# Performance work log

Measured on AMD Instinct MI355X. Metric: run time of the kernel, lower is better.

## Reference

```python
import jax, jax.numpy as jnp
import numpy as np

B, N, DIM = 2, 2048, 512
HEADS, DIM_HEAD = 8, 64
INNER = HEADS * DIM_HEAD  # 512
SCALE = DIM_HEAD ** -0.5


def setup_inputs() -> dict:
    key = jax.random.key(0)
    k1, k2, k3, k4, k5 = jax.random.split(key, 5)
    s = 0.02
    return {
        "x1": jax.random.normal(k1, (B, N, DIM), jnp.float32),
        "x2": jax.random.normal(k2, (B, N, DIM), jnp.float32),
        "W_qk": jax.random.normal(k3, (DIM, 2 * INNER), jnp.float32) * s,
        "W_v": jax.random.normal(k4, (DIM, INNER), jnp.float32) * s,
        "W_out": jax.random.normal(k5, (INNER, DIM), jnp.float32) * s,
        "b_out": jnp.zeros((DIM,), jnp.float32),
    }


def _split_heads(t):
    # [b, n, h*d] -> [b, h, n, d]
    b, n, _ = t.shape
    return t.reshape(b, n, HEADS, DIM_HEAD).transpose(0, 2, 1, 3)


def reference(x1, x2, W_qk, W_v, W_out, b_out):
    # to_qk(x1) -> chunk into k, v ; to_v(x2) -> q  (names in orig are swapped)
    kv = x1 @ W_qk                      # [b, n1, 2*inner]
    k, v = jnp.split(kv, 2, axis=-1)
    q = x2 @ W_v                        # [b, n2, inner]
    q, k, v = _split_heads(q), _split_heads(k), _split_heads(v)  # [b,h,n,d]
    dots = jnp.einsum("bhid,bhjd->bhij", q, k) * SCALE  # [b,h,n2,n1]
    attn = jax.nn.softmax(dots, axis=-1)
    out = jnp.einsum("bhij,bhjd->bhid", attn, v)         # [b,h,n2,d]
    out = out.transpose(0, 2, 1, 3).reshape(out.shape[0], out.shape[2], INNER)
    return out @ W_out + b_out          # [b, n2, dim]
```

## Files before the change

kernel.cpp:

```cpp
#include <hip/hip_runtime.h>

typedef short bf16x8 __attribute__((ext_vector_type(8)));
typedef float f32x4 __attribute__((ext_vector_type(4)));
typedef unsigned short u16;
typedef u16 u16x8 __attribute__((ext_vector_type(8)));
typedef u16 u16x4 __attribute__((ext_vector_type(4)));

#define DEV __device__ __forceinline__

DEV u16 f2bf(float f) {
  unsigned u = __float_as_uint(f);
  u += 0x7fff + ((u >> 16) & 1);
  return (u16)(u >> 16);
}

#define MFMA16(a, b, c) __builtin_amdgcn_mfma_f32_16x16x32_bf16(a, b, c, 0, 0, 0)

__global__ __launch_bounds__(256) void preproc(
    const float* __restrict__ x1, const float* __restrict__ x2,
    const float* __restrict__ Wqk, const float* __restrict__ Wv,
    const float* __restrict__ Wout,
    u16* __restrict__ x1b, u16* __restrict__ x2b,
    u16* __restrict__ WqkT, u16* __restrict__ WvT, u16* __restrict__ WoutT) {
  __shared__ float tf[32][33];
  int bx = blockIdx.x, t = threadIdx.x;
  if (bx < 2048) {
    const float* src = (bx < 1024) ? x1 : x2;
    u16* dst = (bx < 1024) ? x1b : x2b;
    long base = (long)(bx & 1023) * 2048 + t * 8;
    float4 a = *(const float4*)(src + base);
    float4 b = *(const float4*)(src + base + 4);
    u16x8 o;
    o[0] = f2bf(a.x); o[1] = f2bf(a.y); o[2] = f2bf(a.z); o[3] = f2bf(a.w);
    o[4] = f2bf(b.x); o[5] = f2bf(b.y); o[6] = f2bf(b.z); o[7] = f2bf(b.w);
    *(u16x8*)(dst + base) = o;
    return;
  }
  const float* src; u16* dst; int Ncols; int id;
  if (bx < 2560)      { id = bx - 2048; src = Wqk;  dst = WqkT;  Ncols = 1024; }
  else if (bx < 2816) { id = bx - 2560; src = Wv;   dst = WvT;   Ncols = 512;  }
  else                { id = bx - 2816; src = Wout; dst = WoutT; Ncols = 512;  }
  int tilesPerRow = Ncols >> 5;
  int tr = id / tilesPerRow, tc = id % tilesPerRow;
  int r0 = tr * 32, c0 = tc * 32;
  {
    int r = t >> 3, c4 = (t & 7) * 4;
    float4 v = *(const float4*)(src + (long)(r0 + r) * Ncols + c0 + c4);
    tf[r][c4] = v.x; tf[r][c4 + 1] = v.y; tf[r][c4 + 2] = v.z; tf[r][c4 + 3] = v.w;
  }
  __syncthreads();
  {
    int c = t >> 3, r4 = (t & 7) * 4;
    u16x4 o;
    o[0] = f2bf(tf[r4][c]); o[1] = f2bf(tf[r4 + 1][c]);
    o[2] = f2bf(tf[r4 + 2][c]); o[3] = f2bf(tf[r4 + 3][c]);
    *(u16x4*)(dst + (long)(c0 + c) * 512 + r0 + r4) = o;
  }
}

template <int MODE>
__global__ __launch_bounds__(256) void gemm_bf16(
    const u16* __restrict__ A, const u16* __restrict__ BT,
    u16* __restrict__ out_q, u16* __restrict__ out_k, u16* __restrict__ out_v,
    float* __restrict__ out_f, const float* __restrict__ bias) {
  __shared__ u16 sA[2][128 * 40];
  __shared__ u16 sB[2][64 * 40];
  int t = threadIdx.x, bx = blockIdx.x;
  int m0 = (bx & 31) * 128, n0 = (bx >> 5) * 64;
  int w = t >> 6, l = t & 63, lm = l & 15, lq = l >> 4;

  f32x4 zero = {0.f, 0.f, 0.f, 0.f};
  f32x4 acc[2][4];
#pragma unroll
  for (int i = 0; i < 2; ++i)
#pragma unroll
    for (int j = 0; j < 4; ++j) acc[i][j] = zero;

  int sm = t >> 2;
  int skc = (t & 3) * 8;
  const u16* gA = A + (long)(m0 + sm) * 512 + skc;
  const u16* gB = BT + (long)(n0 + sm) * 512 + skc;

  bf16x8 a0 = *(const bf16x8*)(gA);
  bf16x8 a1 = *(const bf16x8*)(gA + (long)64 * 512);
  bf16x8 b0 = *(const bf16x8*)(gB);
  *(bf16x8*)(sA[0] + sm * 40 + skc) = a0;
  *(bf16x8*)(sA[0] + (sm + 64) * 40 + skc) = a1;
  *(bf16x8*)(sB[0] + sm * 40 + skc) = b0;
  __syncthreads();

  for (int kt = 0; kt < 16; ++kt) {
    int cur = kt & 1;
    if (kt < 15) {
      a0 = *(const bf16x8*)(gA + (kt + 1) * 32);
      a1 = *(const bf16x8*)(gA + (long)64 * 512 + (kt + 1) * 32);
      b0 = *(const bf16x8*)(gB + (kt + 1) * 32);
    }
    bf16x8 af[2], bfr[4];
    af[0] = *(const bf16x8*)(sA[cur] + (w * 32 + lm) * 40 + lq * 8);
    af[1] = *(const bf16x8*)(sA[cur] + (w * 32 + 16 + lm) * 40 + lq * 8);
#pragma unroll
    for (int s = 0; s < 4; ++s)
      bfr[s] = *(const bf16x8*)(sB[cur] + (s * 16 + lm) * 40 + lq * 8);
#pragma unroll
    for (int ms = 0; ms < 2; ++ms)
#pragma unroll
      for (int s = 0; s < 4; ++s)
        acc[ms][s] = MFMA16(af[ms], bfr[s], acc[ms][s]);
    if (kt < 15) {
      int nxt = 1 - cur;
      *(bf16x8*)(sA[nxt] + sm * 40 + skc) = a0;
      *(bf16x8*)(sA[nxt] + (sm + 64) * 40 + skc) = a1;
      *(bf16x8*)(sB[nxt] + sm * 40 + skc) = b0;
    }
    __syncthreads();
  }

#pragma unroll
  for (int ms = 0; ms < 2; ++ms) {
    int gmBase = m0 + w * 32 + ms * 16 + lq * 4;
#pragma unroll
    for (int s = 0; s < 4; ++s) {
      int gc = n0 + s * 16 + lm;
#pragma unroll
      for (int r = 0; r < 4; ++r) {
        int gm = gmBase + r;
        float v = acc[ms][s][r];
        if (MODE == 2) {
          out_f[(long)gm * 512 + gc] = v + bias[gc];
        } else if (MODE == 0) {
          int b = gm >> 11, n = gm & 2047;
          out_q[(((long)(b << 3) + (gc >> 6)) * 2048 + n) * 64 + (gc & 63)] =
              f2bf(v * 0.125f);
        } else {
          int b = gm >> 11, n = gm & 2047;
          if (gc < 512)
            out_k[(((long)(b << 3) + (gc >> 6)) * 2048 + n) * 64 + (gc & 63)] = f2bf(v);
          else {
            int c = gc - 512;
            out_v[(((long)(b << 3) + (c >> 6)) * 2048 + n) * 64 + (c & 63)] = f2bf(v);
          }
        }
      }
    }
  }
}

__global__ __launch_bounds__(256) void vtrans(const u16* __restrict__ V,
                                              u16* __restrict__ Vt) {
  __shared__ u16 tile[64][72];
  int nt = blockIdx.x, bh = blockIdx.y;
  const u16* src = V + ((long)bh * 2048 + nt * 64) * 64;
  u16* dst = Vt + (long)bh * 64 * 2048 + nt * 64;
  int t = threadIdx.x;
  int r = t >> 2, c = (t & 3) * 16;
  *(u16x8*)(&tile[r][c]) = *(const u16x8*)(src + (long)r * 64 + c);
  *(u16x8*)(&tile[r][c + 8]) = *(const u16x8*)(src + (long)r * 64 + c + 8);
  __syncthreads();
  int d = t >> 2, n0 = (t & 3) * 16;
  u16x8 o0, o1;
#pragma unroll
  for (int i = 0; i < 8; ++i) {
    o0[i] = tile[n0 + i][d];
    o1[i] = tile[n0 + 8 + i][d];
  }
  *(u16x8*)(dst + (long)d * 2048 + n0) = o0;
  *(u16x8*)(dst + (long)d * 2048 + n0 + 8) = o1;
}

__global__ __launch_bounds__(256) void attn(
    const u16* __restrict__ Q, const u16* __restrict__ K,
    const u16* __restrict__ Vt, u16* __restrict__ O) {
  int qt = blockIdx.x, bh = blockIdx.y;
  int b = bh >> 3, h = bh & 7;
  const u16* Kh = K + (long)bh * 2048 * 64;
  const u16* Vh = Vt + (long)bh * 64 * 2048;
  int t = threadIdx.x, w = t >> 6, l = t & 63, lm = l & 15, lq = l >> 4;

  __shared__ u16 sK[2][64 * 72];
  __shared__ u16 sV[2][64 * 72];
  __shared__ u16 sP[64 * 72];

  bf16x8 qf[2];
  {
    const u16* qptr = Q + (long)bh * 2048 * 64 + (long)(qt * 64 + w * 16 + lm) * 64 + lq * 8;
    qf[0] = *(const bf16x8*)(qptr);
    qf[1] = *(const bf16x8*)(qptr + 32);
  }

  f32x4 zero = {0.f, 0.f, 0.f, 0.f};
  f32x4 accO[4];
#pragma unroll
  for (int s = 0; s < 4; ++s) accO[s] = zero;
  f32x4 lacc = zero;

  int row = t >> 2, c16 = (t & 3) * 16;
  const u16* gK = Kh + (long)row * 64 + c16;
  const u16* gV = Vh + (long)row * 2048 + c16;

  bf16x8 k0 = *(const bf16x8*)(gK);
  bf16x8 k1 = *(const bf16x8*)(gK + 8);
  bf16x8 v0 = *(const bf16x8*)(gV);
  bf16x8 v1 = *(const bf16x8*)(gV + 8);
  *(bf16x8*)(sK[0] + row * 72 + c16) = k0;
  *(bf16x8*)(sK[0] + row * 72 + c16 + 8) = k1;
  *(bf16x8*)(sV[0] + row * 72 + c16) = v0;
  *(bf16x8*)(sV[0] + row * 72 + c16 + 8) = v1;
  __syncthreads();

  for (int jt = 0; jt < 32; ++jt) {
    int cur = jt & 1;
    if (jt < 31) {
      long off = (long)(jt + 1) * 64;
      k0 = *(const bf16x8*)(gK + off * 64);
      k1 = *(const bf16x8*)(gK + off * 64 + 8);
      v0 = *(const bf16x8*)(gV + off);
      v1 = *(const bf16x8*)(gV + off + 8);
    }
    const u16* bK = sK[cur];
    const u16* bV = sV[cur];

    f32x4 sacc[4];
#pragma unroll
    for (int s = 0; s < 4; ++s) sacc[s] = zero;
#pragma unroll
    for (int s = 0; s < 4; ++s) {
      bf16x8 kf0 = *(const bf16x8*)(bK + (s * 16 + lm) * 72 + lq * 8);
      bf16x8 kf1 = *(const bf16x8*)(bK + (s * 16 + lm) * 72 + 32 + lq * 8);
      sacc[s] = MFMA16(qf[0], kf0, sacc[s]);
      sacc[s] = MFMA16(qf[1], kf1, sacc[s]);
    }

    float p[4][4];
#pragma unroll
    for (int s = 0; s < 4; ++s)
#pragma unroll
      for (int r = 0; r < 4; ++r) {
        float e = __expf(sacc[s][r]);
        p[s][r] = e;
        lacc[r] += e;
      }

#pragma unroll
    for (int s = 0; s < 4; ++s)
#pragma unroll
      for (int r = 0; r < 4; ++r)
        sP[(w * 16 + lq * 4 + r) * 72 + s * 16 + lm] = f2bf(p[s][r]);

    bf16x8 pf0 = *(const bf16x8*)(sP + (w * 16 + lm) * 72 + lq * 8);
    bf16x8 pf1 = *(const bf16x8*)(sP + (w * 16 + lm) * 72 + 32 + lq * 8);
#pragma unroll
    for (int s = 0; s < 4; ++s) {
      bf16x8 vf0 = *(const bf16x8*)(bV + (s * 16 + lm) * 72 + lq * 8);
      bf16x8 vf1 = *(const bf16x8*)(bV + (s * 16 + lm) * 72 + 32 + lq * 8);
      accO[s] = MFMA16(pf0, vf0, accO[s]);
      accO[s] = MFMA16(pf1, vf1, accO[s]);
    }

    if (jt < 31) {
      int nxt = 1 - cur;
      *(bf16x8*)(sK[nxt] + row * 72 + c16) = k0;
      *(bf16x8*)(sK[nxt] + row * 72 + c16 + 8) = k1;
      *(bf16x8*)(sV[nxt] + row * 72 + c16) = v0;
      *(bf16x8*)(sV[nxt] + row * 72 + c16 + 8) = v1;
    }
    __syncthreads();
  }

#pragma unroll
  for (int m = 1; m < 16; m <<= 1) {
    lacc[0] += __shfl_xor(lacc[0], m);
    lacc[1] += __shfl_xor(lacc[1], m);
    lacc[2] += __shfl_xor(lacc[2], m);
    lacc[3] += __shfl_xor(lacc[3], m);
  }
  f32x4 inv;
#pragma unroll
  for (int r = 0; r < 4; ++r) inv[r] = 1.f / lacc[r];

#pragma unroll
  for (int s = 0; s < 4; ++s)
#pragma unroll
    for (int r = 0; r < 4; ++r) {
      int n = qt * 64 + w * 16 + lq * 4 + r;
      O[((long)b * 2048 + n) * 512 + h * 64 + s * 16 + lm] = f2bf(accO[s][r] * inv[r]);
    }
}

extern "C" void kernel_launch(void* const* d_in, const int* in_sizes, int n_in,
                              void* d_out, int out_size, void* d_ws, size_t ws_size,
                              hipStream_t stream) {
  const float* x1 = (const float*)d_in[0];
  const float* x2 = (const float*)d_in[1];
  const float* Wqk = (const float*)d_in[2];
  const float* Wv = (const float*)d_in[3];
  const float* Wout = (const float*)d_in[4];
  const float* bout = (const float*)d_in[5];
  float* out = (float*)d_out;

  u16* ws = (u16*)d_ws;
  const long SZ = 2097152;
  u16* Qw = ws;
  u16* Kw = ws + SZ;
  u16* Vw = ws + 2 * SZ;
  u16* Ow = ws + 3 * SZ;
  u16* x1b = ws + 4 * SZ;
  u16* x2b = ws + 5 * SZ;
  u16* Vtw = ws + 6 * SZ;
  u16* WqkT = ws + 7 * SZ;
  u16* WvT = ws + 7 * SZ + 524288;
  u16* WoutT = ws + 7 * SZ + 524288 + 262144;

  preproc<<<3072, 256, 0, stream>>>(x1, x2, Wqk, Wv, Wout, x1b, x2b, WqkT, WvT, WoutT);
  gemm_bf16<0><<<256, 256, 0, stream>>>(x2b, WvT, Qw, nullptr, nullptr, nullptr, nullptr);
  gemm_bf16<1><<<512, 256, 0, stream>>>(x1b, WqkT, nullptr, Kw, Vw, nullptr, nullptr);
  vtrans<<<dim3(32, 16), 256, 0, stream>>>(Vw, Vtw);
  attn<<<dim3(32, 16), 256, 0, stream>>>(Qw, Kw, Vtw, Ow);
  gemm_bf16<2><<<256, 256, 0, stream>>>(Ow, WoutT, nullptr, nullptr, nullptr, out, bout);
}
```

Before: 149.6 us.

## Fuse input conversion and V transpose into GEMMs, rework attention with 32x32 MFMA

The fp32-to-bf16 conversion of x1/x2 moves into the projection GEMM's A-operand loads, dropping a separate conversion pass and its workspace traffic. The KV GEMM writes V already transposed, which removes the vtrans kernel. The attention kernel is rewritten to use 32x32 MFMA tiles with 128-thread blocks and keeps P in registers, using the 32x32x8 MFMA layout or lane shuffles instead of an LDS round-trip. The trade-off is more register pressure and fewer waves per block in attention, plus uncoalesced 4-element strided stores for Vt.

```diff
diff --git a/kernel.cpp b/kernel.cpp
--- a/kernel.cpp
+++ b/kernel.cpp
@@ -1,7 +1,9 @@
 #include <hip/hip_runtime.h>
 
 typedef short bf16x8 __attribute__((ext_vector_type(8)));
+typedef short bf16x4 __attribute__((ext_vector_type(4)));
 typedef float f32x4 __attribute__((ext_vector_type(4)));
+typedef float f32x16 __attribute__((ext_vector_type(16)));
 typedef unsigned short u16;
 typedef u16 u16x8 __attribute__((ext_vector_type(8)));
 typedef u16 u16x4 __attribute__((ext_vector_type(4)));
@@ -14,32 +16,31 @@
   return (u16)(u >> 16);
 }
 
+DEV int pkbf(float lo, float hi) {
+  return __builtin_amdgcn_perm(__float_as_uint(hi) + 0x8000u,
+                               __float_as_uint(lo) + 0x8000u, 0x07060302u);
+}
+
 #define MFMA16(a, b, c) __builtin_amdgcn_mfma_f32_16x16x32_bf16(a, b, c, 0, 0, 0)
-
-__global__ __launch_bounds__(256) void preproc(
-    const float* __restrict__ x1, const float* __restrict__ x2,
+#define MFMA3216(a, b, c) __builtin_amdgcn_mfma_f32_32x32x16_bf16(a, b, c, 0, 0, 0)
+
+#if __has_builtin(__builtin_amdgcn_mfma_f32_32x32x8bf16_1k)
+#define HAVE_PV8 1
+#define PVMFMA(a, b, c) __builtin_amdgcn_mfma_f32_32x32x8bf16_1k(a, b, c, 0, 0, 0)
+#else
+#define HAVE_PV8 0
+#endif
+
+__global__ __launch_bounds__(256) void wprep(
     const float* __restrict__ Wqk, const float* __restrict__ Wv,
     const float* __restrict__ Wout,
-    u16* __restrict__ x1b, u16* __restrict__ x2b,
     u16* __restrict__ WqkT, u16* __restrict__ WvT, u16* __restrict__ WoutT) {
   __shared__ float tf[32][33];
   int bx = blockIdx.x, t = threadIdx.x;
-  if (bx < 2048) {
-    const float* src = (bx < 1024) ? x1 : x2;
-    u16* dst = (bx < 1024) ? x1b : x2b;
-    long base = (long)(bx & 1023) * 2048 + t * 8;
-    float4 a = *(const float4*)(src + base);
-    float4 b = *(const float4*)(src + base + 4);
-    u16x8 o;
-    o[0] = f2bf(a.x); o[1] = f2bf(a.y); o[2] = f2bf(a.z); o[3] = f2bf(a.w);
-    o[4] = f2bf(b.x); o[5] = f2bf(b.y); o[6] = f2bf(b.z); o[7] = f2bf(b.w);
-    *(u16x8*)(dst + base) = o;
-    return;
-  }
   const float* src; u16* dst; int Ncols; int id;
-  if (bx < 2560)      { id = bx - 2048; src = Wqk;  dst = WqkT;  Ncols = 1024; }
-  else if (bx < 2816) { id = bx - 2560; src = Wv;   dst = WvT;   Ncols = 512;  }
-  else                { id = bx - 2816; src = Wout; dst = WoutT; Ncols = 512;  }
+  if (bx < 512)      { id = bx;       src = Wqk;  dst = WqkT;  Ncols = 1024; }
+  else if (bx < 768) { id = bx - 512; src = Wv;   dst = WvT;   Ncols = 512; }
+  else               { id = bx - 768; src = Wout; dst = WoutT; Ncols = 512; }
   int tilesPerRow = Ncols >> 5;
   int tr = id / tilesPerRow, tc = id % tilesPerRow;
   int r0 = tr * 32, c0 = tc * 32;
@@ -59,10 +60,11 @@
 }
 
 template <int MODE>
-__global__ __launch_bounds__(256) void gemm_bf16(
-    const u16* __restrict__ A, const u16* __restrict__ BT,
-    u16* __restrict__ out_q, u16* __restrict__ out_k, u16* __restrict__ out_v,
+__global__ __launch_bounds__(256) void gemm_k(
+    const void* __restrict__ Ap, const u16* __restrict__ BT,
+    u16* __restrict__ out_q, u16* __restrict__ out_k, u16* __restrict__ out_vt,
     float* __restrict__ out_f, const float* __restrict__ bias) {
+  constexpr bool AF32 = (MODE != 2);
   __shared__ u16 sA[2][128 * 40];
   __shared__ u16 sB[2][64 * 40];
   int t = threadIdx.x, bx = blockIdx.x;
@@ -78,11 +80,28 @@
 
   int sm = t >> 2;
   int skc = (t & 3) * 8;
-  const u16* gA = A + (long)(m0 + sm) * 512 + skc;
+  const float* gAf = (const float*)Ap + (long)(m0 + sm) * 512 + skc;
+  const u16* gAh = (const u16*)Ap + (long)(m0 + sm) * 512 + skc;
   const u16* gB = BT + (long)(n0 + sm) * 512 + skc;
 
-  bf16x8 a0 = *(const bf16x8*)(gA);
-  bf16x8 a1 = *(const bf16x8*)(gA + (long)64 * 512);
+  auto loadA = [&](int kt, int rows) {
+    bf16x8 o;
+    long off = (long)rows * 512 + kt * 32;
+    if constexpr (AF32) {
+      float4 f0 = *(const float4*)(gAf + off);
+      float4 f1 = *(const float4*)(gAf + off + 4);
+      o[0] = (short)f2bf(f0.x); o[1] = (short)f2bf(f0.y);
+      o[2] = (short)f2bf(f0.z); o[3] = (short)f2bf(f0.w);
+      o[4] = (short)f2bf(f1.x); o[5] = (short)f2bf(f1.y);
+      o[6] = (short)f2bf(f1.z); o[7] = (short)f2bf(f1.w);
+    } else {
+      o = *(const bf16x8*)(gAh + off);
+    }
+    return o;
+  };
+
+  bf16x8 a0 = loadA(0, 0);
+  bf16x8 a1 = loadA(0, 64);
   bf16x8 b0 = *(const bf16x8*)(gB);
   *(bf16x8*)(sA[0] + sm * 40 + skc) = a0;
   *(bf16x8*)(sA[0] + (sm + 64) * 40 + skc) = a1;
@@ -92,8 +111,8 @@
   for (int kt = 0; kt < 16; ++kt) {
     int cur = kt & 1;
     if (kt < 15) {
-      a0 = *(const bf16x8*)(gA + (kt + 1) * 32);
-      a1 = *(const bf16x8*)(gA + (long)64 * 512 + (kt + 1) * 32);
+      a0 = loadA(kt + 1, 0);
+      a1 = loadA(kt + 1, 64);
       b0 = *(const bf16x8*)(gB + (kt + 1) * 32);
     }
     bf16x8 af[2], bfr[4];
@@ -122,168 +141,166 @@
 #pragma unroll
     for (int s = 0; s < 4; ++s) {
       int gc = n0 + s * 16 + lm;
-#pragma unroll
-      for (int r = 0; r < 4; ++r) {
-        int gm = gmBase + r;
-        float v = acc[ms][s][r];
-        if (MODE == 2) {
-          out_f[(long)gm * 512 + gc] = v + bias[gc];
-        } else if (MODE == 0) {
-          int b = gm >> 11, n = gm & 2047;
-          out_q[(((long)(b << 3) + (gc >> 6)) * 2048 + n) * 64 + (gc & 63)] =
-              f2bf(v * 0.125f);
+      if (MODE == 2) {
+#pragma unroll
+        for (int r = 0; r < 4; ++r)
+          out_f[(long)(gmBase + r) * 512 + gc] = acc[ms][s][r] + bias[gc];
+      } else if (MODE == 0) {
+        int b = gmBase >> 11, n = gmBase & 2047;
+#pragma unroll
+        for (int r = 0; r < 4; ++r)
+          out_q[(((long)(b << 3) + (gc >> 6)) * 2048 + n + r) * 64 + (gc & 63)] =
+              f2bf(acc[ms][s][r] * 0.125f);
+      } else {
+        int b = gmBase >> 11, n = gmBase & 2047;
+        if (gc < 512) {
+#pragma unroll
+          for (int r = 0; r < 4; ++r)
+            out_k[(((long)(b << 3) + (gc >> 6)) * 2048 + n + r) * 64 + (gc & 63)] =
+                f2bf(acc[ms][s][r]);
         } else {
-          int b = gm >> 11, n = gm & 2047;
-          if (gc < 512)
-            out_k[(((long)(b << 3) + (gc >> 6)) * 2048 + n) * 64 + (gc & 63)] = f2bf(v);
-          else {
-            int c = gc - 512;
-            out_v[(((long)(b << 3) + (c >> 6)) * 2048 + n) * 64 + (c & 63)] = f2bf(v);
-          }
+          int c = gc - 512, h = c >> 6, d = c & 63;
+          u16x4 vv;
+#pragma unroll
+          for (int r = 0; r < 4; ++r) vv[r] = f2bf(acc[ms][s][r]);
+          *(u16x4*)(out_vt + (((long)(b << 3) + h) * 64 + d) * 2048 + n) = vv;
         }
       }
     }
   }
 }
 
-__global__ __launch_bounds__(256) void vtrans(const u16* __restrict__ V,
-                                              u16* __restrict__ Vt) {
-  __shared__ u16 tile[64][72];
-  int nt = blockIdx.x, bh = blockIdx.y;
-  const u16* src = V + ((long)bh * 2048 + nt * 64) * 64;
-  u16* dst = Vt + (long)bh * 64 * 2048 + nt * 64;
-  int t = threadIdx.x;
-  int r = t >> 2, c = (t & 3) * 16;
-  *(u16x8*)(&tile[r][c]) = *(const u16x8*)(src + (long)r * 64 + c);
-  *(u16x8*)(&tile[r][c + 8]) = *(const u16x8*)(src + (long)r * 64 + c + 8);
-  __syncthreads();
-  int d = t >> 2, n0 = (t & 3) * 16;
-  u16x8 o0, o1;
-#pragma unroll
-  for (int i = 0; i < 8; ++i) {
-    o0[i] = tile[n0 + i][d];
-    o1[i] = tile[n0 + 8 + i][d];
-  }
-  *(u16x8*)(dst + (long)d * 2048 + n0) = o0;
-  *(u16x8*)(dst + (long)d * 2048 + n0 + 8) = o1;
-}
-
-__global__ __launch_bounds__(256) void attn(
+__global__ __launch_bounds__(128) void attn(
     const u16* __restrict__ Q, const u16* __restrict__ K,
     const u16* __restrict__ Vt, u16* __restrict__ O) {
-  int qt = blockIdx.x, bh = blockIdx.y;
+  int id = blockIdx.x;
+  int bh = id & 15, qt = id >> 4;
   int b = bh >> 3, h = bh & 7;
   const u16* Kh = K + (long)bh * 2048 * 64;
   const u16* Vh = Vt + (long)bh * 64 * 2048;
-  int t = threadIdx.x, w = t >> 6, l = t & 63, lm = l & 15, lq = l >> 4;
+  int t = threadIdx.x, w = t >> 6, lane = t & 63, ln = lane & 31, hi = lane >> 5;
 
   __shared__ u16 sK[2][64 * 72];
   __shared__ u16 sV[2][64 * 72];
-  __shared__ u16 sP[64 * 72];
-
-  bf16x8 qf[2];
+
+  bf16x8 qf[4];
   {
-    const u16* qptr = Q + (long)bh * 2048 * 64 + (long)(qt * 64 + w * 16 + lm) * 64 + lq * 8;
-    qf[0] = *(const bf16x8*)(qptr);
-    qf[1] = *(const bf16x8*)(qptr + 32);
-  }
-
-  f32x4 zero = {0.f, 0.f, 0.f, 0.f};
-  f32x4 accO[4];
-#pragma unroll
-  for (int s = 0; s < 4; ++s) accO[s] = zero;
-  f32x4 lacc = zero;
-
-  int row = t >> 2, c16 = (t & 3) * 16;
-  const u16* gK = Kh + (long)row * 64 + c16;
-  const u16* gV = Vh + (long)row * 2048 + c16;
-
-  bf16x8 k0 = *(const bf16x8*)(gK);
-  bf16x8 k1 = *(const bf16x8*)(gK + 8);
-  bf16x8 v0 = *(const bf16x8*)(gV);
-  bf16x8 v1 = *(const bf16x8*)(gV + 8);
-  *(bf16x8*)(sK[0] + row * 72 + c16) = k0;
-  *(bf16x8*)(sK[0] + row * 72 + c16 + 8) = k1;
-  *(bf16x8*)(sV[0] + row * 72 + c16) = v0;
-  *(bf16x8*)(sV[0] + row * 72 + c16 + 8) = v1;
+    const u16* qp = Q + (long)bh * 2048 * 64 + (long)(qt * 64 + w * 32 + ln) * 64 + hi * 8;
+#pragma unroll
+    for (int dc = 0; dc < 4; ++dc) qf[dc] = *(const bf16x8*)(qp + dc * 16);
+  }
+
+  f32x16 accO[2];
+#pragma unroll
+  for (int dt = 0; dt < 2; ++dt)
+#pragma unroll
+    for (int i = 0; i < 16; ++i) accO[dt][i] = 0.f;
+  float dacc = 0.f;
+
+  int r = t >> 1, half = t & 1;
+  const u16* gK = Kh + (long)r * 64 + half * 32;
+  const u16* gV = Vh + (long)r * 2048 + half * 32;
+  int woff = r * 72 + half * 32;
+
+  bf16x8 kp[4], vp[4];
+#pragma unroll
+  for (int i = 0; i < 4; ++i) {
+    kp[i] = *(const bf16x8*)(gK + i * 8);
+    vp[i] = *(const bf16x8*)(gV + i * 8);
+  }
+#pragma unroll
+  for (int i = 0; i < 4; ++i) {
+    *(bf16x8*)(sK[0] + woff + i * 8) = kp[i];
+    *(bf16x8*)(sV[0] + woff + i * 8) = vp[i];
+  }
   __syncthreads();
 
   for (int jt = 0; jt < 32; ++jt) {
     int cur = jt & 1;
     if (jt < 31) {
-      long off = (long)(jt + 1) * 64;
-      k0 = *(const bf16x8*)(gK + off * 64);
-      k1 = *(const bf16x8*)(gK + off * 64 + 8);
-      v0 = *(const bf16x8*)(gV + off);
-      v1 = *(const bf16x8*)(gV + off + 8);
+      long ko = (long)(jt + 1) * 64 * 64, vo = (long)(jt + 1) * 64;
+#pragma unroll
+      for (int i = 0; i < 4; ++i) {
+        kp[i] = *(const bf16x8*)(gK + ko + i * 8);
+        vp[i] = *(const bf16x8*)(gV + vo + i * 8);
+      }
     }
     const u16* bK = sK[cur];
     const u16* bV = sV[cur];
 
-    f32x4 sacc[4];
-#pragma unroll
-    for (int s = 0; s < 4; ++s) sacc[s] = zero;
-#pragma unroll
-    for (int s = 0; s < 4; ++s) {
-      bf16x8 kf0 = *(const bf16x8*)(bK + (s * 16 + lm) * 72 + lq * 8);
-      bf16x8 kf1 = *(const bf16x8*)(bK + (s * 16 + lm) * 72 + 32 + lq * 8);
-      sacc[s] = MFMA16(qf[0], kf0, sacc[s]);
-      sacc[s] = MFMA16(qf[1], kf1, sacc[s]);
-    }
-
-    float p[4][4];
-#pragma unroll
-    for (int s = 0; s < 4; ++s)
-#pragma unroll
-      for (int r = 0; r < 4; ++r) {
-        float e = __expf(sacc[s][r]);
-        p[s][r] = e;
-        lacc[r] += e;
-      }
-
-#pragma unroll
-    for (int s = 0; s < 4; ++s)
-#pragma unroll
-      for (int r = 0; r < 4; ++r)
-        sP[(w * 16 + lq * 4 + r) * 72 + s * 16 + lm] = f2bf(p[s][r]);
-
-    bf16x8 pf0 = *(const bf16x8*)(sP + (w * 16 + lm) * 72 + lq * 8);
-    bf16x8 pf1 = *(const bf16x8*)(sP + (w * 16 + lm) * 72 + 32 + lq * 8);
-#pragma unroll
-    for (int s = 0; s < 4; ++s) {
-      bf16x8 vf0 = *(const bf16x8*)(bV + (s * 16 + lm) * 72 + lq * 8);
-      bf16x8 vf1 = *(const bf16x8*)(bV + (s * 16 + lm) * 72 + 32 + lq * 8);
-      accO[s] = MFMA16(pf0, vf0, accO[s]);
-      accO[s] = MFMA16(pf1, vf1, accO[s]);
+#pragma unroll
+    for (int kt2 = 0; kt2 < 2; ++kt2) {
+      f32x16 st;
+#pragma unroll
+      for (int i = 0; i < 16; ++i) st[i] = 0.f;
+#pragma unroll
+      for (int dc = 0; dc < 4; ++dc) {
+        bf16x8 kf = *(const bf16x8*)(bK + (kt2 * 32 + ln) * 72 + dc * 16 + hi * 8);
+        st = MFMA3216(kf, qf[dc], st);
+      }
+      float p[16];
+#pragma unroll
+      for (int i = 0; i < 16; ++i) {
+        float e = __expf(st[i]);
+        p[i] = e;
+        dacc += e;
+      }
+#if HAVE_PV8
+#pragma unroll
+      for (int c = 0; c < 4; ++c) {
+        union { int2 i2; bf16x4 v; } u;
+        u.i2.x = pkbf(p[c * 4 + 0], p[c * 4 + 1]);
+        u.i2.y = pkbf(p[c * 4 + 2], p[c * 4 + 3]);
+#pragma unroll
+        for (int dt = 0; dt < 2; ++dt) {
+          bf16x4 vf = *(const bf16x4*)(bV + (dt * 32 + ln) * 72 + kt2 * 32 + c * 8 + hi * 4);
+          accO[dt] = PVMFMA(vf, u.v, accO[dt]);
+        }
+      }
+#else
+#pragma unroll
+      for (int c2 = 0; c2 < 2; ++c2) {
+        int o0x = pkbf(p[c2 * 8 + 0], p[c2 * 8 + 1]);
+        int o0y = pkbf(p[c2 * 8 + 2], p[c2 * 8 + 3]);
+        int o1x = pkbf(p[c2 * 8 + 4], p[c2 * 8 + 5]);
+        int o1y = pkbf(p[c2 * 8 + 6], p[c2 * 8 + 7]);
+        int s0x = __shfl_xor(o0x, 32), s0y = __shfl_xor(o0y, 32);
+        int s1x = __shfl_xor(o1x, 32), s1y = __shfl_xor(o1y, 32);
+        union { int4 i4; bf16x8 v; } u;
+        if (hi) { u.i4.x = s1x; u.i4.y = s1y; u.i4.z = o1x; u.i4.w = o1y; }
+        else    { u.i4.x = o0x; u.i4.y = o0y; u.i4.z = s0x; u.i4.w = s0y; }
+#pragma unroll
+        for (int dt = 0; dt < 2; ++dt) {
+          bf16x8 vf = *(const bf16x8*)(bV + (dt * 32 + ln) * 72 + kt2 * 32 + c2 * 16 + hi * 8);
+          accO[dt] = MFMA3216(vf, u.v, accO[dt]);
+        }
+      }
+#endif
     }
 
     if (jt < 31) {
-      int nxt = 1 - cur;
-      *(bf16x8*)(sK[nxt] + row * 72 + c16) = k0;
-      *(bf16x8*)(sK[nxt] + row * 72 + c16 + 8) = k1;
-      *(bf16x8*)(sV[nxt] + row * 72 + c16) = v0;
-      *(bf16x8*)(sV[nxt] + row * 72 + c16 + 8) = v1;
+      int nxt = cur ^ 1;
+#pragma unroll
+      for (int i = 0; i < 4; ++i) {
+        *(bf16x8*)(sK[nxt] + woff + i * 8) = kp[i];
+        *(bf16x8*)(sV[nxt] + woff + i * 8) = vp[i];
+      }
     }
     __syncthreads();
   }
 
-#pragma unroll
-  for (int m = 1; m < 16; m <<= 1) {
-    lacc[0] += __shfl_xor(lacc[0], m);
-    lacc[1] += __shfl_xor(lacc[1], m);
-    lacc[2] += __shfl_xor(lacc[2], m);
-    lacc[3] += __shfl_xor(lacc[3], m);
-  }
-  f32x4 inv;
-#pragma unroll
-  for (int r = 0; r < 4; ++r) inv[r] = 1.f / lacc[r];
-
-#pragma unroll
-  for (int s = 0; s < 4; ++s)
-#pragma unroll
-    for (int r = 0; r < 4; ++r) {
-      int n = qt * 64 + w * 16 + lq * 4 + r;
-      O[((long)b * 2048 + n) * 512 + h * 64 + s * 16 + lm] = f2bf(accO[s][r] * inv[r]);
+  dacc += __shfl_xor(dacc, 32);
+  float inv = 1.f / dacc;
+
+  u16* Ob = O + ((long)b * 2048 + qt * 64 + w * 32 + ln) * 512 + h * 64;
+#pragma unroll
+  for (int dt = 0; dt < 2; ++dt)
+#pragma unroll
+    for (int g = 0; g < 4; ++g) {
+      u16x4 o;
+#pragma unroll
+      for (int rr = 0; rr < 4; ++rr) o[rr] = f2bf(accO[dt][g * 4 + rr] * inv);
+      *(u16x4*)(Ob + dt * 32 + g * 8 + hi * 4) = o;
     }
 }
 
@@ -302,19 +319,15 @@
   const long SZ = 2097152;
   u16* Qw = ws;
   u16* Kw = ws + SZ;
-  u16* Vw = ws + 2 * SZ;
+  u16* Vtw = ws + 2 * SZ;
   u16* Ow = ws + 3 * SZ;
-  u16* x1b = ws + 4 * SZ;
-  u16* x2b = ws + 5 * SZ;
-  u16* Vtw = ws + 6 * SZ;
-  u16* WqkT = ws + 7 * SZ;
-  u16* WvT = ws + 7 * SZ + 524288;
-  u16* WoutT = ws + 7 * SZ + 524288 + 262144;
-
-  preproc<<<3072, 256, 0, stream>>>(x1, x2, Wqk, Wv, Wout, x1b, x2b, WqkT, WvT, WoutT);
-  gemm_bf16<0><<<256, 256, 0, stream>>>(x2b, WvT, Qw, nullptr, nullptr, nullptr, nullptr);
-  gemm_bf16<1><<<512, 256, 0, stream>>>(x1b, WqkT, nullptr, Kw, Vw, nullptr, nullptr);
-  vtrans<<<dim3(32, 16), 256, 0, stream>>>(Vw, Vtw);
-  attn<<<dim3(32, 16), 256, 0, stream>>>(Qw, Kw, Vtw, Ow);
-  gemm_bf16<2><<<256, 256, 0, stream>>>(Ow, WoutT, nullptr, nullptr, nullptr, out, bout);
-}
+  u16* WqkT = ws + 4 * SZ;
+  u16* WvT = WqkT + 524288;
+  u16* WoutT = WvT + 262144;
+
+  wprep<<<1024, 256, 0, stream>>>(Wqk, Wv, Wout, WqkT, WvT, WoutT);
+  gemm_k<0><<<256, 256, 0, stream>>>(x2, WvT, Qw, nullptr, nullptr, nullptr, nullptr);
+  gemm_k<1><<<512, 256, 0, stream>>>(x1, WqkT, nullptr, Kw, Vtw, nullptr, nullptr);
+  attn<<<512, 128, 0, stream>>>(Qw, Kw, Vtw, Ow);
+  gemm_k<2><<<256, 256, 0, stream>>>(Ow, WoutT, nullptr, nullptr, nullptr, out, bout);
+}
```

After: 145.3 us. 2.9% less time.
